# Optimization experiments

Measured on AMD Instinct MI355X. Metric: run time of the kernel, lower is better.

Reference implementation:

```python
import jax, jax.numpy as jnp
import numpy as np

B, T, E, H = 2, 2048, 1024, 16
D = E // H  # head_dim = 64


def setup_inputs() -> dict:
    key = jax.random.key(0)
    ks = jax.random.split(key, 7)
    s = 1.0 / np.sqrt(E)
    queries = jax.random.normal(ks[0], (B, T, E), dtype=jnp.float32)
    keys = jax.random.normal(ks[1], (B, T, E), dtype=jnp.float32)
    values = jax.random.normal(ks[2], (B, T, E), dtype=jnp.float32)
    # causal mask: True where attention is disallowed (masked_fill semantics)
    mask = jnp.triu(jnp.ones((T, T), dtype=bool), k=1)[None, None]  # [1,1,T,T]
    Wq = jax.random.uniform(ks[3], (E, E), jnp.float32, -s, s)
    Wk = jax.random.uniform(ks[4], (E, E), jnp.float32, -s, s)
    Wv = jax.random.uniform(ks[5], (E, E), jnp.float32, -s, s)
    Wo = jax.random.uniform(ks[6], (E, E), jnp.float32, -s, s)
    return {"queries": queries, "keys": keys, "values": values, "mask": mask,
            "Wq": Wq, "Wk": Wk, "Wv": Wv, "Wo": Wo}


def _split(x):
    # [B,T,E] -> [B,H,T,D]
    return x.reshape(B, T, H, D).transpose(0, 2, 1, 3)


def reference(queries, keys, values, mask, Wq, Wk, Wv, Wo):
    # nn.Linear(E,E,bias=False): y = x @ W.T
    q = _split(queries @ Wq.T)  # [B,H,T,D]
    k = _split(keys @ Wk.T)
    v = _split(values @ Wv.T)
    scores = jnp.einsum('bhqd,bhkd->bhqk', q, k) / jnp.sqrt(jnp.float32(D))
    scores = jnp.where(mask, -jnp.inf, scores)
    weights = jax.nn.softmax(scores, axis=-1)
    attn = jnp.einsum('bhqk,bhkd->bhqd', weights, v)  # [B,H,T,D]
    joined = attn.transpose(0, 2, 1, 3).reshape(B, T, E)
    return joined @ Wo.T
```

## Files before the change

### kernel.cpp

```cpp
#include <hip/hip_runtime.h>
#include <hip/hip_bf16.h>

#define T_DIM 2048
#define E_DIM 1024
#define MM 4096
#define NN 1024
#define KK 1024
#define MSZ ((size_t)MM * KK)
#define WSZ ((size_t)NN * KK)

typedef __attribute__((ext_vector_type(8))) short bh8;
typedef __attribute__((ext_vector_type(4))) short bh4;
typedef __attribute__((ext_vector_type(4))) float fx4;

static __device__ __forceinline__ short f2bf(float f) {
  union { float f; unsigned u; } v; v.f = f;
  unsigned r = (v.u + 0x7fffu + ((v.u >> 16) & 1u)) >> 16;
  return (short)(unsigned short)r;
}

static __device__ __forceinline__ void gload16(const void* g, void* l) {
  __builtin_amdgcn_global_load_lds(
      (const __attribute__((address_space(1))) unsigned*)g,
      (__attribute__((address_space(3))) unsigned*)l, 16, 0, 0);
}

template<int CTRL>
static __device__ __forceinline__ float dppf(float x) {
  union { float f; int i; } a, b;
  a.f = x;
  b.i = __builtin_amdgcn_update_dpp(0, a.i, CTRL, 0xf, 0xf, false);
  return b.f;
}
static __device__ __forceinline__ float rowmax16(float x) {
  x = fmaxf(x, dppf<0x121>(x));
  x = fmaxf(x, dppf<0x122>(x));
  x = fmaxf(x, dppf<0x124>(x));
  x = fmaxf(x, dppf<0x128>(x));
  return x;
}
static __device__ __forceinline__ float rowsum16(float x) {
  x += dppf<0x121>(x);
  x += dppf<0x122>(x);
  x += dppf<0x124>(x);
  x += dppf<0x128>(x);
  return x;
}

__global__ __launch_bounds__(256) void cvt_w(const float* __restrict__ s0,
                                             const float* __restrict__ s1,
                                             const float* __restrict__ s2,
                                             const float* __restrict__ s3,
                                             short* __restrict__ dst) {
  int a = blockIdx.y;
  const float* sp = a == 0 ? s0 : a == 1 ? s1 : a == 2 ? s2 : s3;
  size_t i = ((size_t)blockIdx.x * 256 + threadIdx.x) * 8;
  fx4 x = *(const fx4*)(sp + i);
  fx4 y = *(const fx4*)(sp + i + 4);
  bh8 o;
#pragma unroll
  for (int j = 0; j < 4; j++) { o[j] = f2bf(x[j]); o[4 + j] = f2bf(y[j]); }
  *(bh8*)(dst + (size_t)a * WSZ + i) = o;
}

__global__ __launch_bounds__(256) void cvt_act(const float* __restrict__ s0,
                                               const float* __restrict__ s1,
                                               const float* __restrict__ s2,
                                               short* __restrict__ dst) {
  int a = blockIdx.y;
  const float* sp = a == 0 ? s0 : a == 1 ? s1 : s2;
  size_t i = ((size_t)blockIdx.x * 256 + threadIdx.x) * 8;
  fx4 x = *(const fx4*)(sp + i);
  fx4 y = *(const fx4*)(sp + i + 4);
  bh8 o;
#pragma unroll
  for (int j = 0; j < 4; j++) { o[j] = f2bf(x[j]); o[4 + j] = f2bf(y[j]); }
  *(bh8*)(dst + (size_t)a * MSZ + i) = o;
}

template<bool AF32, bool OUTF32>
__global__ __launch_bounds__(256) void gemm_fast(const void* __restrict__ A0,
                                                 const void* __restrict__ A1,
                                                 const void* __restrict__ A2,
                                                 const short* __restrict__ W0,
                                                 void* __restrict__ C0)
{
  __shared__ short As[128 * 32];
  __shared__ short Bs[128 * 32];
  const int tid = threadIdx.x;
  const int lane = tid & 63, w = tid >> 6;
  const int lm = lane & 15, lg = lane >> 4;
  const int wr = w >> 1, wc = w & 1;
  const int m0 = blockIdx.y * 128, n0 = blockIdx.x * 128;
  const int z = blockIdx.z;
  const void* Ap = z == 0 ? A0 : z == 1 ? A1 : A2;
  const short* W = W0 + (size_t)z * WSZ;

  fx4 acc[4][4] = {};

  for (int k0 = 0; k0 < KK; k0 += 32) {
    __syncthreads();
#pragma unroll
    for (int c = 0; c < 2; c++) {
      int idx = c * 256 + tid;
      int row = idx >> 2, kc = idx & 3;
      gload16(W + (size_t)(n0 + row) * KK + k0 + kc * 8, Bs + idx * 8);
      if constexpr (AF32) {
        const float* Af = (const float*)Ap;
        const float* src = Af + (size_t)(m0 + row) * KK + k0 + kc * 8;
        fx4 x = *(const fx4*)src;
        fx4 y = *(const fx4*)(src + 4);
        bh8 o;
#pragma unroll
        for (int j = 0; j < 4; j++) { o[j] = f2bf(x[j]); o[4 + j] = f2bf(y[j]); }
        *(bh8*)&As[idx * 8] = o;
      } else {
        const short* Ab = (const short*)Ap;
        gload16(Ab + (size_t)(m0 + row) * KK + k0 + kc * 8, As + idx * 8);
      }
    }
    __syncthreads();
    bh8 af[4], bf[4];
#pragma unroll
    for (int mi = 0; mi < 4; mi++)
      af[mi] = *(const bh8*)&As[(wr * 64 + mi * 16 + lm) * 32 + lg * 8];
#pragma unroll
    for (int ni = 0; ni < 4; ni++)
      bf[ni] = *(const bh8*)&Bs[(wc * 64 + ni * 16 + lm) * 32 + lg * 8];
#pragma unroll
    for (int mi = 0; mi < 4; mi++)
#pragma unroll
      for (int ni = 0; ni < 4; ni++)
        acc[mi][ni] = __builtin_amdgcn_mfma_f32_16x16x32_bf16(af[mi], bf[ni], acc[mi][ni], 0, 0, 0);
  }

#pragma unroll
  for (int mi = 0; mi < 4; mi++)
#pragma unroll
    for (int ni = 0; ni < 4; ni++) {
      int row = m0 + wr * 64 + mi * 16 + lg * 4;
      int col = n0 + wc * 64 + ni * 16 + lm;
#pragma unroll
      for (int r = 0; r < 4; r++) {
        float vv = acc[mi][ni][r];
        if constexpr (OUTF32) ((float*)C0)[(size_t)z * MSZ + (size_t)(row + r) * NN + col] = vv;
        else ((short*)C0)[(size_t)z * MSZ + (size_t)(row + r) * NN + col] = f2bf(vv);
      }
    }
}

__global__ __launch_bounds__(256) void gemm_out64(const short* __restrict__ A,
                                                  const short* __restrict__ W,
                                                  float* __restrict__ C)
{
  __shared__ short As[64 * 32];
  __shared__ short Bs[128 * 32];
  const int tid = threadIdx.x;
  const int lane = tid & 63, w = tid >> 6;
  const int lm = lane & 15, lg = lane >> 4;
  const int lin = blockIdx.x + 8 * blockIdx.y;
  const int swz = (lin & 7) * 64 + (lin >> 3);
  const int n0 = (swz & 7) * 128, m0 = (swz >> 3) * 64;

  fx4 acc[4][2] = {};

  for (int k0 = 0; k0 < KK; k0 += 32) {
    __syncthreads();
    {
      int row = tid >> 2, kc = tid & 3;
      gload16(A + (size_t)(m0 + row) * KK + k0 + kc * 8, As + tid * 8);
#pragma unroll
      for (int c = 0; c < 2; c++) {
        int idx = c * 256 + tid;
        int brow = idx >> 2, bkc = idx & 3;
        gload16(W + (size_t)(n0 + brow) * KK + k0 + bkc * 8, Bs + idx * 8);
      }
    }
    __syncthreads();
    bh8 af[4], bf[2];
#pragma unroll
    for (int mi = 0; mi < 4; mi++)
      af[mi] = *(const bh8*)&As[(mi * 16 + lm) * 32 + lg * 8];
#pragma unroll
    for (int ni = 0; ni < 2; ni++)
      bf[ni] = *(const bh8*)&Bs[(w * 32 + ni * 16 + lm) * 32 + lg * 8];
#pragma unroll
    for (int mi = 0; mi < 4; mi++)
#pragma unroll
      for (int ni = 0; ni < 2; ni++)
        acc[mi][ni] = __builtin_amdgcn_mfma_f32_16x16x32_bf16(af[mi], bf[ni], acc[mi][ni], 0, 0, 0);
  }

#pragma unroll
  for (int mi = 0; mi < 4; mi++)
#pragma unroll
    for (int ni = 0; ni < 2; ni++) {
      int row = m0 + mi * 16 + lg * 4;
      int col = n0 + w * 32 + ni * 16 + lm;
#pragma unroll
      for (int r = 0; r < 4; r++)
        C[(size_t)(row + r) * NN + col] = acc[mi][ni][r];
    }
}

template<bool AF32, bool OUTF32>
__global__ __launch_bounds__(256) void gemm_nt(const void* __restrict__ Ap,
                                               const float* __restrict__ Bw,
                                               void* __restrict__ Cp,
                                               int M, int N, int K)
{
  __shared__ short As[128 * 40];
  __shared__ short Bs[128 * 40];
  const int tid = threadIdx.x;
  const int lane = tid & 63;
  const int w = tid >> 6;
  const int lm = lane & 15;
  const int lg = lane >> 4;
  const int wr = w >> 1, wc = w & 1;
  const int m0 = blockIdx.y * 128, n0 = blockIdx.x * 128;

  fx4 acc[4][4] = {};

  for (int k0 = 0; k0 < K; k0 += 32) {
    __syncthreads();
#pragma unroll
    for (int i = 0; i < 4; ++i) {
      int g = i * 256 + tid;
      int row = g >> 3, cg = g & 7;
      bh4 a4;
      if constexpr (AF32) {
        const float* A = (const float*)Ap;
        fx4 v = *(const fx4*)(A + (size_t)(m0 + row) * K + k0 + cg * 4);
#pragma unroll
        for (int j = 0; j < 4; j++) a4[j] = f2bf(v[j]);
      } else {
        const short* A = (const short*)Ap;
        a4 = *(const bh4*)(A + (size_t)(m0 + row) * K + k0 + cg * 4);
      }
      *(bh4*)&As[row * 40 + cg * 4] = a4;

      fx4 bv = *(const fx4*)(Bw + (size_t)(n0 + row) * K + k0 + cg * 4);
      bh4 b4;
#pragma unroll
      for (int j = 0; j < 4; j++) b4[j] = f2bf(bv[j]);
      *(bh4*)&Bs[row * 40 + cg * 4] = b4;
    }
    __syncthreads();

    bh8 af[4], bf[4];
#pragma unroll
    for (int mi = 0; mi < 4; mi++)
      af[mi] = *(const bh8*)&As[(wr * 64 + mi * 16 + lm) * 40 + lg * 8];
#pragma unroll
    for (int ni = 0; ni < 4; ni++)
      bf[ni] = *(const bh8*)&Bs[(wc * 64 + ni * 16 + lm) * 40 + lg * 8];
#pragma unroll
    for (int mi = 0; mi < 4; mi++)
#pragma unroll
      for (int ni = 0; ni < 4; ni++)
        acc[mi][ni] = __builtin_amdgcn_mfma_f32_16x16x32_bf16(af[mi], bf[ni], acc[mi][ni], 0, 0, 0);
  }

#pragma unroll
  for (int mi = 0; mi < 4; mi++) {
#pragma unroll
    for (int ni = 0; ni < 4; ni++) {
      int row = m0 + wr * 64 + mi * 16 + lg * 4;
      int col = n0 + wc * 64 + ni * 16 + lm;
#pragma unroll
      for (int r = 0; r < 4; r++) {
        float vv = acc[mi][ni][r];
        if constexpr (OUTF32) ((float*)Cp)[(size_t)(row + r) * N + col] = vv;
        else        ((short*)Cp)[(size_t)(row + r) * N + col] = f2bf(vv);
      }
    }
  }
}

__global__ __launch_bounds__(256) void attn_kernel(const short* __restrict__ Q,
                                                   const short* __restrict__ Kb,
                                                   const short* __restrict__ Vb,
                                                   short* __restrict__ At)
{
  __shared__ short Kl[2][64 * 64];
  __shared__ short Vt[2][64 * 64];
  __shared__ short Pl[4 * 16 * 72];

  const int tid = threadIdx.x;
  const int lane = tid & 63;
  const int w = tid >> 6;
  const int lm = lane & 15;
  const int lg = lane >> 4;
  const int lin = blockIdx.x + 16 * blockIdx.y;
  const int swz = (lin & 7) * 64 + (lin >> 3);
  const int pi = swz & 15;
  const int bh = swz >> 4;
  const size_t headoff = (size_t)(bh >> 4) * T_DIM * E_DIM + (size_t)(bh & 15) * 64;

  const float SCALE2 = 0.125f * 1.44269504f;

  const int r0 = tid >> 3, ch0 = tid & 7;
  const int r1 = (256 + tid) >> 3, ch1 = tid & 7;

  for (int s = 0; s < 2; s++) {
    const int qt = s ? (31 - pi) : pi;
    const int q0 = qt * 64;

    const int qrow = q0 + w * 16 + lm;
    bh8 qf[2];
#pragma unroll
    for (int ks = 0; ks < 2; ks++)
      qf[ks] = *(const bh8*)(Q + headoff + (size_t)qrow * E_DIM + ks * 32 + lg * 8);

    fx4 oacc[4] = {};
    float m_r[4], l_r[4];
#pragma unroll
    for (int r = 0; r < 4; r++) { m_r[r] = -INFINITY; l_r[r] = 0.0f; }

    {
      gload16(Kb + headoff + (size_t)r0 * E_DIM + ((ch0 ^ (r0 & 7)) * 8), &Kl[0][tid * 8]);
      gload16(Kb + headoff + (size_t)r1 * E_DIM + ((ch1 ^ (r1 & 7)) * 8), &Kl[0][(256 + tid) * 8]);
      bh8 v8a = *(const bh8*)(Vb + headoff + (size_t)r0 * E_DIM + ch0 * 8);
      bh8 v8b = *(const bh8*)(Vb + headoff + (size_t)r1 * E_DIM + ch1 * 8);
#pragma unroll
      for (int j = 0; j < 8; j++) {
        int d = ch0 * 8 + j;
        Vt[0][d * 64 + (((r0 >> 3) ^ ((ch0 + j) & 7)) * 8) + (r0 & 7)] = v8a[j];
        Vt[0][d * 64 + (((r1 >> 3) ^ ((ch1 + j) & 7)) * 8) + (r1 & 7)] = v8b[j];
      }
    }
    __syncthreads();

    int cur = 0;
    for (int t = 0; t <= qt; ++t) {
      const bool pre = (t < qt);
      bh8 v8a, v8b;
      if (pre) {
        const int kvn = (t + 1) * 64;
        gload16(Kb + headoff + (size_t)(kvn + r0) * E_DIM + ((ch0 ^ (r0 & 7)) * 8),
                &Kl[cur ^ 1][tid * 8]);
        gload16(Kb + headoff + (size_t)(kvn + r1) * E_DIM + ((ch1 ^ (r1 & 7)) * 8),
                &Kl[cur ^ 1][(256 + tid) * 8]);
        v8a = *(const bh8*)(Vb + headoff + (size_t)(kvn + r0) * E_DIM + ch0 * 8);
        v8b = *(const bh8*)(Vb + headoff + (size_t)(kvn + r1) * E_DIM + ch1 * 8);
      }

      fx4 sacc[4] = {};
#pragma unroll
      for (int nb = 0; nb < 4; nb++) {
        const int rK = nb * 16 + lm;
#pragma unroll
        for (int ks = 0; ks < 2; ks++) {
          bh8 kf = *(const bh8*)&Kl[cur][rK * 64 + (((ks * 4 + lg) ^ (lm & 7)) * 8)];
          sacc[nb] = __builtin_amdgcn_mfma_f32_16x16x32_bf16(qf[ks], kf, sacc[nb], 0, 0, 0);
        }
      }

      float sv[4][4];
      const bool maskt = (t == qt);
#pragma unroll
      for (int nb = 0; nb < 4; nb++)
#pragma unroll
        for (int r = 0; r < 4; r++) {
          float x = sacc[nb][r] * SCALE2;
          if (maskt && (nb * 16 + lm > w * 16 + lg * 4 + r)) x = -INFINITY;
          sv[nb][r] = x;
        }

      float p[4][4];
#pragma unroll
      for (int r = 0; r < 4; r++) {
        float rm = fmaxf(fmaxf(sv[0][r], sv[1][r]), fmaxf(sv[2][r], sv[3][r]));
        rm = rowmax16(rm);
        float mn = fmaxf(m_r[r], rm);
        float fac = exp2f(m_r[r] - mn);
        float ps = 0.0f;
#pragma unroll
        for (int nb = 0; nb < 4; nb++) { p[nb][r] = exp2f(sv[nb][r] - mn); ps += p[nb][r]; }
        ps = rowsum16(ps);
        l_r[r] = l_r[r] * fac + ps;
        m_r[r] = mn;
#pragma unroll
        for (int db = 0; db < 4; db++) oacc[db][r] *= fac;
      }

#pragma unroll
      for (int nb = 0; nb < 4; nb++)
#pragma unroll
        for (int r = 0; r < 4; r++)
          Pl[w * 1152 + (lg * 4 + r) * 72 + nb * 16 + lm] = f2bf(p[nb][r]);

      bh8 pa[2];
#pragma unroll
      for (int ks = 0; ks < 2; ks++)
        pa[ks] = *(const bh8*)&Pl[w * 1152 + lm * 72 + ks * 32 + lg * 8];
#pragma unroll
      for (int db = 0; db < 4; db++) {
        const int d = db * 16 + lm;
        const int gsw = ((d >> 3) + (d & 7)) & 7;
#pragma unroll
        for (int ks = 0; ks < 2; ks++) {
          bh8 vf = *(const bh8*)&Vt[cur][d * 64 + (((ks * 4 + lg) ^ gsw) * 8)];
          oacc[db] = __builtin_amdgcn_mfma_f32_16x16x32_bf16(pa[ks], vf, oacc[db], 0, 0, 0);
        }
      }

      if (pre) {
#pragma unroll
        for (int j = 0; j < 8; j++) {
          int d = ch0 * 8 + j;
          Vt[cur ^ 1][d * 64 + (((r0 >> 3) ^ ((ch0 + j) & 7)) * 8) + (r0 & 7)] = v8a[j];
          Vt[cur ^ 1][d * 64 + (((r1 >> 3) ^ ((ch1 + j) & 7)) * 8) + (r1 & 7)] = v8b[j];
        }
      }
      __syncthreads();
      cur ^= 1;
    }

#pragma unroll
    for (int r = 0; r < 4; r++) {
      float rl = 1.0f / l_r[r];
      int row = q0 + w * 16 + lg * 4 + r;
#pragma unroll
      for (int db = 0; db < 4; db++)
        At[headoff + (size_t)row * E_DIM + db * 16 + lm] = f2bf(oacc[db][r] * rl);
    }
  }
}

extern "C" void kernel_launch(void* const* d_in, const int* in_sizes, int n_in,
                              void* d_out, int out_size, void* d_ws, size_t ws_size,
                              hipStream_t stream)
{
  const float* q  = (const float*)d_in[0];
  const float* k  = (const float*)d_in[1];
  const float* v  = (const float*)d_in[2];
  const float* Wq = (const float*)d_in[4];
  const float* Wk = (const float*)d_in[5];
  const float* Wv = (const float*)d_in[6];
  const float* Wo = (const float*)d_in[7];

  short* Qb  = (short*)d_ws;
  short* Kbb = Qb + MSZ;
  short* Vbb = Kbb + MSZ;
  short* wqb = Vbb + MSZ;
  short* Xq  = wqb + 4 * WSZ;
  short* At  = Xq;

  const size_t need_full = (3 * MSZ + 4 * WSZ + 3 * MSZ) * 2;
  const size_t need_mid  = (4 * MSZ + 4 * WSZ) * 2;

  if (ws_size >= need_full) {
    cvt_act<<<dim3(MSZ / (256 * 8), 3), 256, 0, stream>>>(q, k, v, Xq);
    cvt_w<<<dim3(WSZ / (256 * 8), 4), 256, 0, stream>>>(Wq, Wk, Wv, Wo, wqb);
    gemm_fast<false, false><<<dim3(NN / 128, MM / 128, 3), 256, 0, stream>>>(
        Xq, Xq + MSZ, Xq + 2 * MSZ, wqb, Qb);
    attn_kernel<<<dim3(16, 32), 256, 0, stream>>>(Qb, Kbb, Vbb, At);
    gemm_out64<<<dim3(NN / 128, MM / 64), 256, 0, stream>>>(
        At, wqb + 3 * WSZ, (float*)d_out);
  } else if (ws_size >= need_mid) {
    short* At2  = Vbb + MSZ;
    short* wqb2 = At2 + MSZ;
    cvt_w<<<dim3(WSZ / (256 * 8), 4), 256, 0, stream>>>(Wq, Wk, Wv, Wo, wqb2);
    gemm_fast<true, false><<<dim3(NN / 128, MM / 128, 3), 256, 0, stream>>>(q, k, v, wqb2, Qb);
    attn_kernel<<<dim3(16, 32), 256, 0, stream>>>(Qb, Kbb, Vbb, At2);
    gemm_out64<<<dim3(NN / 128, MM / 64), 256, 0, stream>>>(
        At2, wqb2 + 3 * WSZ, (float*)d_out);
  } else {
    short* At2 = Vbb + MSZ;
    dim3 gg(NN / 128, MM / 128);
    gemm_nt<true, false><<<gg, 256, 0, stream>>>(q, Wq, Qb, MM, NN, KK);
    gemm_nt<true, false><<<gg, 256, 0, stream>>>(k, Wk, Kbb, MM, NN, KK);
    gemm_nt<true, false><<<gg, 256, 0, stream>>>(v, Wv, Vbb, MM, NN, KK);
    attn_kernel<<<dim3(16, 32), 256, 0, stream>>>(Qb, Kbb, Vbb, At2);
    gemm_nt<false, true><<<gg, 256, 0, stream>>>(At2, Wo, d_out, MM, NN, KK);
  }
}
```

Measured before the change: 251.5 us.

## Fold softmax scale into Wq, split attention into per-tile blocks, skip rescale

The softmax scale times log2(e) is folded into the bf16 conversion of Wq, so the attention kernel no longer multiplies the scores. The attention grid changes from 512 blocks that each process a paired short and long query tile to 1024 blocks of one tile each, launched longest-first. K/V double buffering is dropped in favour of single buffers with two barriers per iteration. The online-softmax rescale is skipped when no row max grows. The GEMM block order is remapped and the mid-workspace path is removed. Losing the K/V prefetch may expose load latency, and folding the scale into bf16 Wq changes rounding slightly.

```diff
diff --git a/kernel.cpp b/kernel.cpp
--- a/kernel.cpp
+++ b/kernel.cpp
@@ -13,6 +13,8 @@
 typedef __attribute__((ext_vector_type(4))) short bh4;
 typedef __attribute__((ext_vector_type(4))) float fx4;
 
+#define QSCALE 0.18033688f
+
 static __device__ __forceinline__ short f2bf(float f) {
   union { float f; unsigned u; } v; v.f = f;
   unsigned r = (v.u + 0x7fffu + ((v.u >> 16) & 1u)) >> 16;
@@ -54,12 +56,13 @@
                                              short* __restrict__ dst) {
   int a = blockIdx.y;
   const float* sp = a == 0 ? s0 : a == 1 ? s1 : a == 2 ? s2 : s3;
+  const float sc = (a == 0) ? QSCALE : 1.0f;
   size_t i = ((size_t)blockIdx.x * 256 + threadIdx.x) * 8;
   fx4 x = *(const fx4*)(sp + i);
   fx4 y = *(const fx4*)(sp + i + 4);
   bh8 o;
 #pragma unroll
-  for (int j = 0; j < 4; j++) { o[j] = f2bf(x[j]); o[4 + j] = f2bf(y[j]); }
+  for (int j = 0; j < 4; j++) { o[j] = f2bf(x[j] * sc); o[4 + j] = f2bf(y[j] * sc); }
   *(bh8*)(dst + (size_t)a * WSZ + i) = o;
 }
 
@@ -78,10 +81,10 @@
   *(bh8*)(dst + (size_t)a * MSZ + i) = o;
 }
 
-template<bool AF32, bool OUTF32>
-__global__ __launch_bounds__(256) void gemm_fast(const void* __restrict__ A0,
-                                                 const void* __restrict__ A1,
-                                                 const void* __restrict__ A2,
+template<bool OUTF32>
+__global__ __launch_bounds__(256) void gemm_fast(const short* __restrict__ A0,
+                                                 const short* __restrict__ A1,
+                                                 const short* __restrict__ A2,
                                                  const short* __restrict__ W0,
                                                  void* __restrict__ C0)
 {
@@ -91,9 +94,11 @@
   const int lane = tid & 63, w = tid >> 6;
   const int lm = lane & 15, lg = lane >> 4;
   const int wr = w >> 1, wc = w & 1;
-  const int m0 = blockIdx.y * 128, n0 = blockIdx.x * 128;
+  const int mb = blockIdx.x * 4 + (blockIdx.y & 3);
+  const int nb = blockIdx.y >> 2;
+  const int m0 = mb * 128, n0 = nb * 128;
   const int z = blockIdx.z;
-  const void* Ap = z == 0 ? A0 : z == 1 ? A1 : A2;
+  const short* Ab = z == 0 ? A0 : z == 1 ? A1 : A2;
   const short* W = W0 + (size_t)z * WSZ;
 
   fx4 acc[4][4] = {};
@@ -105,19 +110,7 @@
       int idx = c * 256 + tid;
       int row = idx >> 2, kc = idx & 3;
       gload16(W + (size_t)(n0 + row) * KK + k0 + kc * 8, Bs + idx * 8);
-      if constexpr (AF32) {
-        const float* Af = (const float*)Ap;
-        const float* src = Af + (size_t)(m0 + row) * KK + k0 + kc * 8;
-        fx4 x = *(const fx4*)src;
-        fx4 y = *(const fx4*)(src + 4);
-        bh8 o;
-#pragma unroll
-        for (int j = 0; j < 4; j++) { o[j] = f2bf(x[j]); o[4 + j] = f2bf(y[j]); }
-        *(bh8*)&As[idx * 8] = o;
-      } else {
-        const short* Ab = (const short*)Ap;
-        gload16(Ab + (size_t)(m0 + row) * KK + k0 + kc * 8, As + idx * 8);
-      }
+      gload16(Ab + (size_t)(m0 + row) * KK + k0 + kc * 8, As + idx * 8);
     }
     __syncthreads();
     bh8 af[4], bf[4];
@@ -277,13 +270,14 @@
   }
 }
 
+template<bool PRESCALED>
 __global__ __launch_bounds__(256) void attn_kernel(const short* __restrict__ Q,
                                                    const short* __restrict__ Kb,
                                                    const short* __restrict__ Vb,
                                                    short* __restrict__ At)
 {
-  __shared__ short Kl[2][64 * 64];
-  __shared__ short Vt[2][64 * 64];
+  __shared__ short Kl[64 * 64];
+  __shared__ short Vt[64 * 64];
   __shared__ short Pl[4 * 16 * 72];
 
   const int tid = threadIdx.x;
@@ -291,140 +285,124 @@
   const int w = tid >> 6;
   const int lm = lane & 15;
   const int lg = lane >> 4;
-  const int lin = blockIdx.x + 16 * blockIdx.y;
-  const int swz = (lin & 7) * 64 + (lin >> 3);
-  const int pi = swz & 15;
-  const int bh = swz >> 4;
+  const int lin = blockIdx.x;
+  const int qt = 31 - (lin >> 5);
+  const int bh = (lin & 7) * 4 + ((lin >> 3) & 3);
   const size_t headoff = (size_t)(bh >> 4) * T_DIM * E_DIM + (size_t)(bh & 15) * 64;
-
-  const float SCALE2 = 0.125f * 1.44269504f;
+  const int q0 = qt * 64;
 
   const int r0 = tid >> 3, ch0 = tid & 7;
   const int r1 = (256 + tid) >> 3, ch1 = tid & 7;
 
-  for (int s = 0; s < 2; s++) {
-    const int qt = s ? (31 - pi) : pi;
-    const int q0 = qt * 64;
-
-    const int qrow = q0 + w * 16 + lm;
-    bh8 qf[2];
-#pragma unroll
-    for (int ks = 0; ks < 2; ks++)
-      qf[ks] = *(const bh8*)(Q + headoff + (size_t)qrow * E_DIM + ks * 32 + lg * 8);
-
-    fx4 oacc[4] = {};
-    float m_r[4], l_r[4];
-#pragma unroll
-    for (int r = 0; r < 4; r++) { m_r[r] = -INFINITY; l_r[r] = 0.0f; }
-
+  const int qrow = q0 + w * 16 + lm;
+  bh8 qf[2];
+#pragma unroll
+  for (int ks = 0; ks < 2; ks++)
+    qf[ks] = *(const bh8*)(Q + headoff + (size_t)qrow * E_DIM + ks * 32 + lg * 8);
+
+  fx4 oacc[4] = {};
+  float m_r[4], l_r[4];
+#pragma unroll
+  for (int r = 0; r < 4; r++) { m_r[r] = -INFINITY; l_r[r] = 0.0f; }
+
+  for (int t = 0; t <= qt; ++t) {
+    const int kv0 = t * 64;
+    if (t) __syncthreads();
+    gload16(Kb + headoff + (size_t)(kv0 + r0) * E_DIM + ((ch0 ^ (r0 & 7)) * 8), &Kl[tid * 8]);
+    gload16(Kb + headoff + (size_t)(kv0 + r1) * E_DIM + ((ch1 ^ (r1 & 7)) * 8), &Kl[(256 + tid) * 8]);
     {
-      gload16(Kb + headoff + (size_t)r0 * E_DIM + ((ch0 ^ (r0 & 7)) * 8), &Kl[0][tid * 8]);
-      gload16(Kb + headoff + (size_t)r1 * E_DIM + ((ch1 ^ (r1 & 7)) * 8), &Kl[0][(256 + tid) * 8]);
-      bh8 v8a = *(const bh8*)(Vb + headoff + (size_t)r0 * E_DIM + ch0 * 8);
-      bh8 v8b = *(const bh8*)(Vb + headoff + (size_t)r1 * E_DIM + ch1 * 8);
+      bh8 v8a = *(const bh8*)(Vb + headoff + (size_t)(kv0 + r0) * E_DIM + ch0 * 8);
+      bh8 v8b = *(const bh8*)(Vb + headoff + (size_t)(kv0 + r1) * E_DIM + ch1 * 8);
 #pragma unroll
       for (int j = 0; j < 8; j++) {
         int d = ch0 * 8 + j;
-        Vt[0][d * 64 + (((r0 >> 3) ^ ((ch0 + j) & 7)) * 8) + (r0 & 7)] = v8a[j];
-        Vt[0][d * 64 + (((r1 >> 3) ^ ((ch1 + j) & 7)) * 8) + (r1 & 7)] = v8b[j];
-      }
-    }
-    __syncthreads();
-
-    int cur = 0;
-    for (int t = 0; t <= qt; ++t) {
-      const bool pre = (t < qt);
-      bh8 v8a, v8b;
-      if (pre) {
-        const int kvn = (t + 1) * 64;
-        gload16(Kb + headoff + (size_t)(kvn + r0) * E_DIM + ((ch0 ^ (r0 & 7)) * 8),
-                &Kl[cur ^ 1][tid * 8]);
-        gload16(Kb + headoff + (size_t)(kvn + r1) * E_DIM + ((ch1 ^ (r1 & 7)) * 8),
-                &Kl[cur ^ 1][(256 + tid) * 8]);
-        v8a = *(const bh8*)(Vb + headoff + (size_t)(kvn + r0) * E_DIM + ch0 * 8);
-        v8b = *(const bh8*)(Vb + headoff + (size_t)(kvn + r1) * E_DIM + ch1 * 8);
-      }
-
-      fx4 sacc[4] = {};
-#pragma unroll
-      for (int nb = 0; nb < 4; nb++) {
-        const int rK = nb * 16 + lm;
-#pragma unroll
-        for (int ks = 0; ks < 2; ks++) {
-          bh8 kf = *(const bh8*)&Kl[cur][rK * 64 + (((ks * 4 + lg) ^ (lm & 7)) * 8)];
-          sacc[nb] = __builtin_amdgcn_mfma_f32_16x16x32_bf16(qf[ks], kf, sacc[nb], 0, 0, 0);
-        }
-      }
-
-      float sv[4][4];
-      const bool maskt = (t == qt);
-#pragma unroll
-      for (int nb = 0; nb < 4; nb++)
-#pragma unroll
-        for (int r = 0; r < 4; r++) {
-          float x = sacc[nb][r] * SCALE2;
-          if (maskt && (nb * 16 + lm > w * 16 + lg * 4 + r)) x = -INFINITY;
-          sv[nb][r] = x;
-        }
-
-      float p[4][4];
+        Vt[d * 64 + (((r0 >> 3) ^ ((ch0 + j) & 7)) * 8) + (r0 & 7)] = v8a[j];
+        Vt[d * 64 + (((r1 >> 3) ^ ((ch1 + j) & 7)) * 8) + (r1 & 7)] = v8b[j];
+      }
+    }
+    __syncthreads();
+
+    fx4 sacc[4] = {};
+#pragma unroll
+    for (int nb = 0; nb < 4; nb++) {
+      const int rK = nb * 16 + lm;
+#pragma unroll
+      for (int ks = 0; ks < 2; ks++) {
+        bh8 kf = *(const bh8*)&Kl[rK * 64 + (((ks * 4 + lg) ^ (lm & 7)) * 8)];
+        sacc[nb] = __builtin_amdgcn_mfma_f32_16x16x32_bf16(qf[ks], kf, sacc[nb], 0, 0, 0);
+      }
+    }
+
+    float sv[4][4];
+    const bool maskt = (t == qt);
+#pragma unroll
+    for (int nb = 0; nb < 4; nb++)
 #pragma unroll
       for (int r = 0; r < 4; r++) {
-        float rm = fmaxf(fmaxf(sv[0][r], sv[1][r]), fmaxf(sv[2][r], sv[3][r]));
-        rm = rowmax16(rm);
-        float mn = fmaxf(m_r[r], rm);
+        float x = PRESCALED ? sacc[nb][r] : sacc[nb][r] * QSCALE;
+        if (maskt && (nb * 16 + lm > w * 16 + lg * 4 + r)) x = -INFINITY;
+        sv[nb][r] = x;
+      }
+
+    float rm4[4];
+    bool stable = true;
+#pragma unroll
+    for (int r = 0; r < 4; r++) {
+      float rm = fmaxf(fmaxf(sv[0][r], sv[1][r]), fmaxf(sv[2][r], sv[3][r]));
+      rm = rowmax16(rm);
+      rm4[r] = rm;
+      stable = stable && (rm <= m_r[r]);
+    }
+    if (!__all(stable)) {
+#pragma unroll
+      for (int r = 0; r < 4; r++) {
+        float mn = fmaxf(m_r[r], rm4[r]);
         float fac = exp2f(m_r[r] - mn);
-        float ps = 0.0f;
-#pragma unroll
-        for (int nb = 0; nb < 4; nb++) { p[nb][r] = exp2f(sv[nb][r] - mn); ps += p[nb][r]; }
-        ps = rowsum16(ps);
-        l_r[r] = l_r[r] * fac + ps;
+        l_r[r] *= fac;
         m_r[r] = mn;
 #pragma unroll
         for (int db = 0; db < 4; db++) oacc[db][r] *= fac;
       }
-
-#pragma unroll
-      for (int nb = 0; nb < 4; nb++)
-#pragma unroll
-        for (int r = 0; r < 4; r++)
-          Pl[w * 1152 + (lg * 4 + r) * 72 + nb * 16 + lm] = f2bf(p[nb][r]);
-
-      bh8 pa[2];
-#pragma unroll
-      for (int ks = 0; ks < 2; ks++)
-        pa[ks] = *(const bh8*)&Pl[w * 1152 + lm * 72 + ks * 32 + lg * 8];
-#pragma unroll
-      for (int db = 0; db < 4; db++) {
-        const int d = db * 16 + lm;
-        const int gsw = ((d >> 3) + (d & 7)) & 7;
-#pragma unroll
-        for (int ks = 0; ks < 2; ks++) {
-          bh8 vf = *(const bh8*)&Vt[cur][d * 64 + (((ks * 4 + lg) ^ gsw) * 8)];
-          oacc[db] = __builtin_amdgcn_mfma_f32_16x16x32_bf16(pa[ks], vf, oacc[db], 0, 0, 0);
-        }
-      }
-
-      if (pre) {
-#pragma unroll
-        for (int j = 0; j < 8; j++) {
-          int d = ch0 * 8 + j;
-          Vt[cur ^ 1][d * 64 + (((r0 >> 3) ^ ((ch0 + j) & 7)) * 8) + (r0 & 7)] = v8a[j];
-          Vt[cur ^ 1][d * 64 + (((r1 >> 3) ^ ((ch1 + j) & 7)) * 8) + (r1 & 7)] = v8b[j];
-        }
-      }
-      __syncthreads();
-      cur ^= 1;
-    }
-
+    }
+    float p[4][4];
 #pragma unroll
     for (int r = 0; r < 4; r++) {
-      float rl = 1.0f / l_r[r];
-      int row = q0 + w * 16 + lg * 4 + r;
-#pragma unroll
-      for (int db = 0; db < 4; db++)
-        At[headoff + (size_t)row * E_DIM + db * 16 + lm] = f2bf(oacc[db][r] * rl);
-    }
+      float ps = 0.0f;
+#pragma unroll
+      for (int nb = 0; nb < 4; nb++) { p[nb][r] = exp2f(sv[nb][r] - m_r[r]); ps += p[nb][r]; }
+      ps = rowsum16(ps);
+      l_r[r] += ps;
+    }
+
+#pragma unroll
+    for (int nb = 0; nb < 4; nb++)
+#pragma unroll
+      for (int r = 0; r < 4; r++)
+        Pl[w * 1152 + (lg * 4 + r) * 72 + nb * 16 + lm] = f2bf(p[nb][r]);
+
+    bh8 pa[2];
+#pragma unroll
+    for (int ks = 0; ks < 2; ks++)
+      pa[ks] = *(const bh8*)&Pl[w * 1152 + lm * 72 + ks * 32 + lg * 8];
+#pragma unroll
+    for (int db = 0; db < 4; db++) {
+      const int d = db * 16 + lm;
+      const int gsw = ((d >> 3) + (d & 7)) & 7;
+#pragma unroll
+      for (int ks = 0; ks < 2; ks++) {
+        bh8 vf = *(const bh8*)&Vt[d * 64 + (((ks * 4 + lg) ^ gsw) * 8)];
+        oacc[db] = __builtin_amdgcn_mfma_f32_16x16x32_bf16(pa[ks], vf, oacc[db], 0, 0, 0);
+      }
+    }
+  }
+
+#pragma unroll
+  for (int r = 0; r < 4; r++) {
+    float rl = 1.0f / l_r[r];
+    int row = q0 + w * 16 + lg * 4 + r;
+#pragma unroll
+    for (int db = 0; db < 4; db++)
+      At[headoff + (size_t)row * E_DIM + db * 16 + lm] = f2bf(oacc[db][r] * rl);
   }
 }
 
@@ -448,31 +426,22 @@
   short* At  = Xq;
 
   const size_t need_full = (3 * MSZ + 4 * WSZ + 3 * MSZ) * 2;
-  const size_t need_mid  = (4 * MSZ + 4 * WSZ) * 2;
 
   if (ws_size >= need_full) {
     cvt_act<<<dim3(MSZ / (256 * 8), 3), 256, 0, stream>>>(q, k, v, Xq);
     cvt_w<<<dim3(WSZ / (256 * 8), 4), 256, 0, stream>>>(Wq, Wk, Wv, Wo, wqb);
-    gemm_fast<false, false><<<dim3(NN / 128, MM / 128, 3), 256, 0, stream>>>(
+    gemm_fast<false><<<dim3(8, 32, 3), 256, 0, stream>>>(
         Xq, Xq + MSZ, Xq + 2 * MSZ, wqb, Qb);
-    attn_kernel<<<dim3(16, 32), 256, 0, stream>>>(Qb, Kbb, Vbb, At);
+    attn_kernel<true><<<1024, 256, 0, stream>>>(Qb, Kbb, Vbb, At);
     gemm_out64<<<dim3(NN / 128, MM / 64), 256, 0, stream>>>(
         At, wqb + 3 * WSZ, (float*)d_out);
-  } else if (ws_size >= need_mid) {
-    short* At2  = Vbb + MSZ;
-    short* wqb2 = At2 + MSZ;
-    cvt_w<<<dim3(WSZ / (256 * 8), 4), 256, 0, stream>>>(Wq, Wk, Wv, Wo, wqb2);
-    gemm_fast<true, false><<<dim3(NN / 128, MM / 128, 3), 256, 0, stream>>>(q, k, v, wqb2, Qb);
-    attn_kernel<<<dim3(16, 32), 256, 0, stream>>>(Qb, Kbb, Vbb, At2);
-    gemm_out64<<<dim3(NN / 128, MM / 64), 256, 0, stream>>>(
-        At2, wqb2 + 3 * WSZ, (float*)d_out);
   } else {
     short* At2 = Vbb + MSZ;
     dim3 gg(NN / 128, MM / 128);
     gemm_nt<true, false><<<gg, 256, 0, stream>>>(q, Wq, Qb, MM, NN, KK);
     gemm_nt<true, false><<<gg, 256, 0, stream>>>(k, Wk, Kbb, MM, NN, KK);
     gemm_nt<true, false><<<gg, 256, 0, stream>>>(v, Wv, Vbb, MM, NN, KK);
-    attn_kernel<<<dim3(16, 32), 256, 0, stream>>>(Qb, Kbb, Vbb, At2);
+    attn_kernel<false><<<1024, 256, 0, stream>>>(Qb, Kbb, Vbb, At2);
     gemm_nt<false, true><<<gg, 256, 0, stream>>>(At2, Wo, d_out, MM, NN, KK);
   }
 }
```

Measured after the change: 242.2 us. 3.7% less time.
